# Kernel optimization log

Measured on AMD Instinct MI355X. Metric: run time of the kernel, lower is better.

The kernel has to match this reference:

```python
import jax, jax.numpy as jnp
import numpy as np

B, S, NX, NH = 2, 2048, 1024, 16
HD = NX // NH  # head dim = 64

def setup_inputs() -> dict:
    key = jax.random.key(0)
    k1, k2, k3 = jax.random.split(key, 3)
    return {
        "x": jax.random.normal(k1, (B, S, NX), dtype=jnp.float32),
        "c_attn_w": jax.random.normal(k2, (NX, 3 * NX), dtype=jnp.float32) * 0.02,
        "c_attn_b": jnp.zeros((3 * NX,), dtype=jnp.float32),
        "c_proj_w": jax.random.normal(k3, (NX, NX), dtype=jnp.float32) * 0.02,
        "c_proj_b": jnp.zeros((NX,), dtype=jnp.float32),
    }

def reference(x, c_attn_w, c_attn_b, c_proj_w, c_proj_b):
    b, s, nx = x.shape
    # fused QKV projection (Conv1D == affine on last dim)
    qkv = x @ c_attn_w + c_attn_b                      # [b, s, 3*nx]
    q, k, v = jnp.split(qkv, 3, axis=-1)
    # split heads -> [b, h, s, d]
    q = q.reshape(b, s, NH, HD).transpose(0, 2, 1, 3)
    k = k.reshape(b, s, NH, HD).transpose(0, 2, 1, 3)
    v = v.reshape(b, s, NH, HD).transpose(0, 2, 1, 3)
    # scaled scores with causal mask (masked_fill -1e10, matching original)
    w = jnp.einsum("bhqd,bhkd->bhqk", q, k) / jnp.sqrt(jnp.float32(HD))
    causal = jnp.tril(jnp.ones((s, s), dtype=bool))    # [s, s]
    w = jnp.where(causal[None, None, :, :], w, jnp.float32(-1e10))
    w = jax.nn.softmax(w, axis=-1)
    a = jnp.einsum("bhqk,bhkd->bhqd", w, v)            # [b, h, s, d]
    # merge heads
    a = a.transpose(0, 2, 1, 3).reshape(b, s, nx)
    # output projection (dropout is identity in eval)
    return a @ c_proj_w + c_proj_b
```

## Files before the change

kernel.cpp:

```cpp
#include <hip/hip_runtime.h>
#include <cstdint>

typedef unsigned short u16;
typedef unsigned int u32;
typedef float f32x4 __attribute__((ext_vector_type(4)));
typedef __bf16 bf16x8 __attribute__((ext_vector_type(8)));
typedef __bf16 bf16x4 __attribute__((ext_vector_type(4)));
typedef u16 u16x8 __attribute__((ext_vector_type(8)));

#define B_ 2
#define S_ 2048
#define NX_ 1024
#define NH_ 16
#define HD_ 64
#define T3_ 3072
#define M_ 4096
#define SCL 0.18033688011112042f

__device__ __forceinline__ u16 bfbits(float f) {
    __bf16 h = (__bf16)f;
    return __builtin_bit_cast(u16, h);
}

__device__ __forceinline__ void gload_lds16(const void* g, void* l) {
    auto gp = reinterpret_cast<const __attribute__((address_space(1))) u32*>(
        reinterpret_cast<uintptr_t>(g));
    auto lp = reinterpret_cast<__attribute__((address_space(3))) u32*>(
        reinterpret_cast<uintptr_t>(l));
    __builtin_amdgcn_global_load_lds(gp, lp, 16, 0, 0);
}

__global__ __launch_bounds__(256) void cvt_bf16_kernel(const float* __restrict__ X,
                                                       u16* __restrict__ Y) {
    int i = (blockIdx.x * 256 + threadIdx.x) * 4;
    float4 v = *reinterpret_cast<const float4*>(X + i);
    bf16x4 o;
    o[0] = (__bf16)v.x; o[1] = (__bf16)v.y; o[2] = (__bf16)v.z; o[3] = (__bf16)v.w;
    *reinterpret_cast<bf16x4*>(Y + i) = o;
}

__global__ __launch_bounds__(256) void transpose_cvt_kernel(const float* __restrict__ W,
                                                            u16* __restrict__ WT,
                                                            int K, int N) {
    __shared__ float tile[32][33];
    int nbx = N >> 5;
    int nb = (blockIdx.x % nbx) << 5;
    int kb = (blockIdx.x / nbx) << 5;
    int tx = threadIdx.x & 31, ty = threadIdx.x >> 5;
#pragma unroll
    for (int i = 0; i < 32; i += 8)
        tile[ty + i][tx] = W[(size_t)(kb + ty + i) * N + nb + tx];
    __syncthreads();
#pragma unroll
    for (int i = 0; i < 32; i += 8)
        WT[(size_t)(nb + ty + i) * K + kb + tx] = bfbits(tile[tx][ty + i]);
}

#define BM 128
#define BN 128
#define BK 64
__global__ __launch_bounds__(256) void gemm_bt_kernel(const u16* __restrict__ A,
                                                      const u16* __restrict__ Bt,
                                                      const float* __restrict__ bias,
                                                      u16* __restrict__ Cb,
                                                      float* __restrict__ Cf,
                                                      u16* __restrict__ Vt,
                                                      int vcol0,
                                                      int M, int N, int K) {
    __shared__ u16 a_lds[2][BM * BK];
    __shared__ u16 b_lds[2][BN * BK];
    int nbn = N / BN;
    int nwg = gridDim.x;
    int orig = blockIdx.x;
    int wg = (orig & 7) * (nwg >> 3) + (orig >> 3);
    int bm = wg / nbn, bn = wg % nbn;
    int t = threadIdx.x;
    int w = t >> 6, l = t & 63, lg = l >> 4, lr = l & 15;
    int wr = w >> 1, wc = w & 1;
    const u16* Abase = A + (size_t)bm * BM * K;
    const u16* Bbase = Bt + (size_t)bn * BN * K;

    f32x4 zero4 = {0.f, 0.f, 0.f, 0.f};
    f32x4 acc[4][4];
#pragma unroll
    for (int m = 0; m < 4; ++m)
#pragma unroll
        for (int n = 0; n < 4; ++n) acc[m][n] = zero4;

    auto stage = [&](int kt, int bs) {
#pragma unroll
        for (int it = 0; it < 4; ++it) {
            int idx = it * 256 + t;
            int row = idx >> 3, ck = idx & 7;
            int cds = ck ^ (row & 7);
            int ubase = (it * 256 + w * 64) * 8;
            gload_lds16(Abase + (size_t)row * K + kt * BK + cds * 8, &a_lds[bs][ubase]);
            gload_lds16(Bbase + (size_t)row * K + kt * BK + cds * 8, &b_lds[bs][ubase]);
        }
    };

    stage(0, 0);
    __syncthreads();

    int nkt = K / BK;
    for (int kt = 0; kt < nkt; ++kt) {
        int cur = kt & 1;
        if (kt + 1 < nkt) stage(kt + 1, cur ^ 1);

#pragma unroll
        for (int ks = 0; ks < 2; ++ks) {
            int ck = (ks * 4 + lg) ^ (lr & 7);
            bf16x8 af[4], bf[4];
#pragma unroll
            for (int m = 0; m < 4; ++m)
                af[m] = *reinterpret_cast<const bf16x8*>(
                    &a_lds[cur][(wr * 64 + m * 16 + lr) * BK + ck * 8]);
#pragma unroll
            for (int n = 0; n < 4; ++n)
                bf[n] = *reinterpret_cast<const bf16x8*>(
                    &b_lds[cur][(wc * 64 + n * 16 + lr) * BK + ck * 8]);
            __builtin_amdgcn_s_setprio(1);
#pragma unroll
            for (int m = 0; m < 4; ++m)
#pragma unroll
                for (int n = 0; n < 4; ++n)
                    acc[m][n] = __builtin_amdgcn_mfma_f32_16x16x32_bf16(
                        af[m], bf[n], acc[m][n], 0, 0, 0);
            __builtin_amdgcn_s_setprio(0);
        }
        __syncthreads();
    }

#pragma unroll
    for (int n = 0; n < 4; ++n) {
        int col0 = bn * BN + wc * 64 + n * 16;
        int col = col0 + lr;
        float bv = bias[col];
        bool isv = (Vt != nullptr) && (col0 >= vcol0);
#pragma unroll
        for (int m = 0; m < 4; ++m) {
            int row0 = bm * BM + wr * 64 + m * 16 + lg * 4;
            if (isv) {
                int nv = col - vcol0, hh = nv >> 6, dd = nv & 63;
                int bb = row0 >> 11, ss = row0 & 2047;
                bf16x4 pk;
#pragma unroll
                for (int r = 0; r < 4; ++r) pk[r] = (__bf16)(acc[m][n][r] + bv);
                *reinterpret_cast<bf16x4*>(
                    Vt + (((size_t)(bb * 16 + hh) * 64 + dd) << 11) + ss) = pk;
            } else {
#pragma unroll
                for (int r = 0; r < 4; ++r) {
                    float v = acc[m][n][r] + bv;
                    if (Cf) Cf[(size_t)(row0 + r) * N + col] = v;
                    else    Cb[(size_t)(row0 + r) * N + col] = bfbits(v);
                }
            }
        }
    }
}

__global__ __launch_bounds__(256) void attn_kernel(const u16* __restrict__ qkv,
                                                   const u16* __restrict__ Vt,
                                                   u16* __restrict__ outa) {
    __shared__ u16 k_lds[2][4096];
    __shared__ u16 v_lds[2][4096];
    __shared__ u16 p_lds[4096];

    int bid = blockIdx.x;
    int g = bid & 31;
    int j = bid >> 5;
    int j0 = j & 7, kk = j >> 3;
    int qt = (kk == 0) ? j0 : (kk == 1) ? (31 - j0) : (kk == 2) ? (8 + j0) : (23 - j0);
    int b = g >> 4, h = g & 15;
    int t = threadIdx.x, w = t >> 6, l = t & 63, lg = l >> 4, lr = l & 15;
    const u16* base = qkv + (size_t)b * S_ * T3_;
    const u16* vbase = Vt + (size_t)g * 64 * S_;
    int prow = w * 16 + lr;
    int srow = w * 8 + (l >> 3);
    int qb = qt * 64;
    int qrow = qb + w * 16 + lr;

    auto stage = [&](int kt2, int bs) {
        int kb2 = kt2 * 64;
#pragma unroll
        for (int it = 0; it < 2; ++it) {
            int row = it * 32 + srow;
            int ckg = (l & 7) ^ (row & 7);
            gload_lds16(base + (size_t)(kb2 + row) * T3_ + NX_ + h * 64 + ckg * 8,
                        &k_lds[bs][(it * 32 + w * 8) * 64]);
            gload_lds16(vbase + (size_t)row * S_ + kb2 + ckg * 8,
                        &v_lds[bs][(it * 32 + w * 8) * 64]);
        }
    };

    f32x4 zero4 = {0.f, 0.f, 0.f, 0.f};

    bf16x8 qf[2];
#pragma unroll
    for (int ks = 0; ks < 2; ++ks)
        qf[ks] = *reinterpret_cast<const bf16x8*>(
            base + (size_t)qrow * T3_ + h * 64 + ks * 32 + lg * 8);

    f32x4 oacc[4];
#pragma unroll
    for (int dc = 0; dc < 4; ++dc) oacc[dc] = zero4;
    float mrun = -1e30f, lrun = 0.f;
    int nkt = qt + 1;

    stage(0, 0);
    __syncthreads();

    for (int kt = 0; kt < nkt; ++kt) {
        int cur = kt & 1;
        if (kt + 1 < nkt) stage(kt + 1, cur ^ 1);

        f32x4 sacc[4];
#pragma unroll
        for (int kn = 0; kn < 4; ++kn) sacc[kn] = zero4;
        __builtin_amdgcn_s_setprio(1);
#pragma unroll
        for (int ks = 0; ks < 2; ++ks) {
#pragma unroll
            for (int kn = 0; kn < 4; ++kn) {
                bf16x8 kf = *reinterpret_cast<const bf16x8*>(
                    &k_lds[cur][(kn * 16 + lr) * 64 + (((ks * 4 + lg) ^ (lr & 7)) * 8)]);
                sacc[kn] = __builtin_amdgcn_mfma_f32_16x16x32_bf16(
                    kf, qf[ks], sacc[kn], 0, 0, 0);
            }
        }
        __builtin_amdgcn_s_setprio(0);

        if (kt == qt) {
            int qloc = w * 16 + lr;
#pragma unroll
            for (int kn = 0; kn < 4; ++kn)
#pragma unroll
                for (int r = 0; r < 4; ++r)
                    if (kn * 16 + lg * 4 + r > qloc) sacc[kn][r] = -1e30f;
        }

        float mx = -1e30f;
#pragma unroll
        for (int kn = 0; kn < 4; ++kn) {
            float a0 = fmaxf(sacc[kn][0], sacc[kn][1]);
            float a1 = fmaxf(sacc[kn][2], sacc[kn][3]);
            mx = fmaxf(mx, fmaxf(a0, a1));
        }
        mx = fmaxf(mx, __shfl_xor(mx, 16));
        mx = fmaxf(mx, __shfl_xor(mx, 32));

        bool noresc = __all(mx <= mrun + 8.0f);
        float mnew = noresc ? mrun : fmaxf(mrun, mx);

        float rs = 0.f;
#pragma unroll
        for (int kn = 0; kn < 4; ++kn)
#pragma unroll
            for (int r = 0; r < 4; ++r) {
                float pv = exp2f((sacc[kn][r] - mnew) * SCL);
                sacc[kn][r] = pv;
                rs += pv;
            }
        rs += __shfl_xor(rs, 16);
        rs += __shfl_xor(rs, 32);

        if (noresc) {
            lrun += rs;
        } else {
            float fsc = exp2f((mrun - mnew) * SCL);
            mrun = mnew;
            lrun = lrun * fsc + rs;
            float f0 = __shfl(fsc, lg * 4 + 0);
            float f1 = __shfl(fsc, lg * 4 + 1);
            float f2 = __shfl(fsc, lg * 4 + 2);
            float f3 = __shfl(fsc, lg * 4 + 3);
#pragma unroll
            for (int dc = 0; dc < 4; ++dc) {
                oacc[dc][0] *= f0; oacc[dc][1] *= f1;
                oacc[dc][2] *= f2; oacc[dc][3] *= f3;
            }
        }

#pragma unroll
        for (int kn = 0; kn < 4; ++kn) {
            bf16x4 pb;
            pb[0] = (__bf16)sacc[kn][0]; pb[1] = (__bf16)sacc[kn][1];
            pb[2] = (__bf16)sacc[kn][2]; pb[3] = (__bf16)sacc[kn][3];
            int byteoff = prow * 128 + (((2 * kn + (lg >> 1)) ^ (prow & 7)) * 16) + (lg & 1) * 8;
            *reinterpret_cast<bf16x4*>(reinterpret_cast<char*>(p_lds) + byteoff) = pb;
        }

        __builtin_amdgcn_s_setprio(1);
#pragma unroll
        for (int ks = 0; ks < 2; ++ks) {
            bf16x8 pf = *reinterpret_cast<const bf16x8*>(
                reinterpret_cast<char*>(p_lds) + prow * 128 + (((ks * 4 + lg) ^ (prow & 7)) * 16));
#pragma unroll
            for (int dc = 0; dc < 4; ++dc) {
                bf16x8 vf = *reinterpret_cast<const bf16x8*>(
                    &v_lds[cur][(dc * 16 + lr) * 64 + (((ks * 4 + lg) ^ (lr & 7)) * 8)]);
                oacc[dc] = __builtin_amdgcn_mfma_f32_16x16x32_bf16(
                    pf, vf, oacc[dc], 0, 0, 0);
            }
        }
        __builtin_amdgcn_s_setprio(0);
        __syncthreads();
    }

    float inv = 1.f / lrun;
    float i0 = __shfl(inv, lg * 4 + 0);
    float i1 = __shfl(inv, lg * 4 + 1);
    float i2 = __shfl(inv, lg * 4 + 2);
    float i3 = __shfl(inv, lg * 4 + 3);
    u16* ob = outa + (size_t)b * S_ * NX_;
#pragma unroll
    for (int r = 0; r < 4; ++r) {
        float ir = (r == 0) ? i0 : (r == 1) ? i1 : (r == 2) ? i2 : i3;
        int row = qb + w * 16 + lg * 4 + r;
#pragma unroll
        for (int dc = 0; dc < 4; ++dc)
            ob[(size_t)row * NX_ + h * 64 + dc * 16 + lr] = bfbits(oacc[dc][r] * ir);
    }
}

extern "C" void kernel_launch(void* const* d_in, const int* in_sizes, int n_in,
                              void* d_out, int out_size, void* d_ws, size_t ws_size,
                              hipStream_t stream) {
    const float* x        = (const float*)d_in[0];
    const float* c_attn_w = (const float*)d_in[1];
    const float* c_attn_b = (const float*)d_in[2];
    const float* c_proj_w = (const float*)d_in[3];
    const float* c_proj_b = (const float*)d_in[4];
    float* out = (float*)d_out;

    u16* xb     = (u16*)d_ws;
    u16* wqkvT  = xb + (size_t)M_ * NX_;
    u16* wprojT = wqkvT + (size_t)T3_ * NX_;
    u16* qkv    = wprojT + (size_t)NX_ * NX_;
    u16* attno  = xb;
    u16* Vtp    = (u16*)d_out;

    cvt_bf16_kernel<<<(M_ * NX_) / 1024, 256, 0, stream>>>(x, xb);
    transpose_cvt_kernel<<<(T3_ / 32) * (NX_ / 32), 256, 0, stream>>>(c_attn_w, wqkvT, NX_, T3_);
    transpose_cvt_kernel<<<(NX_ / 32) * (NX_ / 32), 256, 0, stream>>>(c_proj_w, wprojT, NX_, NX_);
    gemm_bt_kernel<<<(M_ / BM) * (T3_ / BN), 256, 0, stream>>>(
        xb, wqkvT, c_attn_b, qkv, nullptr, Vtp, 2 * NX_, M_, T3_, NX_);
    attn_kernel<<<1024, 256, 0, stream>>>(qkv, Vtp, attno);
    gemm_bt_kernel<<<(M_ / BM) * (NX_ / BN), 256, 0, stream>>>(
        attno, wprojT, c_proj_b, nullptr, out, nullptr, 0, M_, NX_, NX_);
}
```

Baseline: 121.3 us.

## Load V fragments directly from global and fold softmax scale into Q

Drops the LDS staging of V in the attention kernel. Each lane now loads its V MFMA fragments straight from the pre-transposed global V buffer into registers at the start of every key tile, and the v_lds buffers go away. Separately, the QKV GEMM epilogue multiplies the Q columns by the log2e/sqrt(d) scale, so the softmax loop no longer multiplies each score by the scale. The lazy-rescale threshold is tightened from 8 to 1.5 to keep it in the same units now that scores are pre-scaled. The trade is more global/L2 traffic and register pressure in the attention loop in exchange for less LDS use, fewer VALU ops and higher occupancy, plus a small extra bf16 rounding on Q.

Result: slower. 142.2 us (+17.2%).

```diff
diff --git a/kernel.cpp b/kernel.cpp
--- a/kernel.cpp
+++ b/kernel.cpp
@@ -65,7 +65,7 @@
                                                       u16* __restrict__ Cb,
                                                       float* __restrict__ Cf,
                                                       u16* __restrict__ Vt,
-                                                      int vcol0,
+                                                      int vcol0, int qcols,
                                                       int M, int N, int K) {
     __shared__ u16 a_lds[2][BM * BK];
     __shared__ u16 b_lds[2][BN * BK];
@@ -136,6 +136,7 @@
         int col0 = bn * BN + wc * 64 + n * 16;
         int col = col0 + lr;
         float bv = bias[col];
+        float sc = (col0 < qcols) ? SCL : 1.0f;
         bool isv = (Vt != nullptr) && (col0 >= vcol0);
 #pragma unroll
         for (int m = 0; m < 4; ++m) {
@@ -151,7 +152,7 @@
             } else {
 #pragma unroll
                 for (int r = 0; r < 4; ++r) {
-                    float v = acc[m][n][r] + bv;
+                    float v = (acc[m][n][r] + bv) * sc;
                     if (Cf) Cf[(size_t)(row0 + r) * N + col] = v;
                     else    Cb[(size_t)(row0 + r) * N + col] = bfbits(v);
                 }
@@ -164,7 +165,6 @@
                                                    const u16* __restrict__ Vt,
                                                    u16* __restrict__ outa) {
     __shared__ u16 k_lds[2][4096];
-    __shared__ u16 v_lds[2][4096];
     __shared__ u16 p_lds[4096];
 
     int bid = blockIdx.x;
@@ -180,6 +180,7 @@
     int srow = w * 8 + (l >> 3);
     int qb = qt * 64;
     int qrow = qb + w * 16 + lr;
+    const u16* vptr = vbase + (size_t)lr * S_ + lg * 8;
 
     auto stage = [&](int kt2, int bs) {
         int kb2 = kt2 * 64;
@@ -189,8 +190,6 @@
             int ckg = (l & 7) ^ (row & 7);
             gload_lds16(base + (size_t)(kb2 + row) * T3_ + NX_ + h * 64 + ckg * 8,
                         &k_lds[bs][(it * 32 + w * 8) * 64]);
-            gload_lds16(vbase + (size_t)row * S_ + kb2 + ckg * 8,
-                        &v_lds[bs][(it * 32 + w * 8) * 64]);
         }
     };
 
@@ -213,6 +212,16 @@
 
     for (int kt = 0; kt < nkt; ++kt) {
         int cur = kt & 1;
+        int kb = kt * 64;
+
+        bf16x8 vf[2][4];
+#pragma unroll
+        for (int ks = 0; ks < 2; ++ks)
+#pragma unroll
+            for (int dc = 0; dc < 4; ++dc)
+                vf[ks][dc] = *reinterpret_cast<const bf16x8*>(
+                    vptr + (size_t)(dc * 16) * S_ + kb + ks * 32);
+
         if (kt + 1 < nkt) stage(kt + 1, cur ^ 1);
 
         f32x4 sacc[4];
@@ -250,7 +259,7 @@
         mx = fmaxf(mx, __shfl_xor(mx, 16));
         mx = fmaxf(mx, __shfl_xor(mx, 32));
 
-        bool noresc = __all(mx <= mrun + 8.0f);
+        bool noresc = __all(mx <= mrun + 1.5f);
         float mnew = noresc ? mrun : fmaxf(mrun, mx);
 
         float rs = 0.f;
@@ -258,7 +267,7 @@
         for (int kn = 0; kn < 4; ++kn)
 #pragma unroll
             for (int r = 0; r < 4; ++r) {
-                float pv = exp2f((sacc[kn][r] - mnew) * SCL);
+                float pv = exp2f(sacc[kn][r] - mnew);
                 sacc[kn][r] = pv;
                 rs += pv;
             }
@@ -268,7 +277,7 @@
         if (noresc) {
             lrun += rs;
         } else {
-            float fsc = exp2f((mrun - mnew) * SCL);
+            float fsc = exp2f(mrun - mnew);
             mrun = mnew;
             lrun = lrun * fsc + rs;
             float f0 = __shfl(fsc, lg * 4 + 0);
@@ -297,12 +306,9 @@
             bf16x8 pf = *reinterpret_cast<const bf16x8*>(
                 reinterpret_cast<char*>(p_lds) + prow * 128 + (((ks * 4 + lg) ^ (prow & 7)) * 16));
 #pragma unroll
-            for (int dc = 0; dc < 4; ++dc) {
-                bf16x8 vf = *reinterpret_cast<const bf16x8*>(
-                    &v_lds[cur][(dc * 16 + lr) * 64 + (((ks * 4 + lg) ^ (lr & 7)) * 8)]);
+            for (int dc = 0; dc < 4; ++dc)
                 oacc[dc] = __builtin_amdgcn_mfma_f32_16x16x32_bf16(
-                    pf, vf, oacc[dc], 0, 0, 0);
-            }
+                    pf, vf[ks][dc], oacc[dc], 0, 0, 0);
         }
         __builtin_amdgcn_s_setprio(0);
         __syncthreads();
@@ -345,8 +351,8 @@
     transpose_cvt_kernel<<<(T3_ / 32) * (NX_ / 32), 256, 0, stream>>>(c_attn_w, wqkvT, NX_, T3_);
     transpose_cvt_kernel<<<(NX_ / 32) * (NX_ / 32), 256, 0, stream>>>(c_proj_w, wprojT, NX_, NX_);
     gemm_bt_kernel<<<(M_ / BM) * (T3_ / BN), 256, 0, stream>>>(
-        xb, wqkvT, c_attn_b, qkv, nullptr, Vtp, 2 * NX_, M_, T3_, NX_);
+        xb, wqkvT, c_attn_b, qkv, nullptr, Vtp, 2 * NX_, NX_, M_, T3_, NX_);
     attn_kernel<<<1024, 256, 0, stream>>>(qkv, Vtp, attno);
     gemm_bt_kernel<<<(M_ / BM) * (NX_ / BN), 256, 0, stream>>>(
-        attno, wprojT, c_proj_b, nullptr, out, nullptr, 0, M_, NX_, NX_);
-}
+        attno, wprojT, c_proj_b, nullptr, out, nullptr, 0, 0, M_, NX_, NX_);
+}
```
